# Kernel optimization log

Hardware: AMD Instinct MI355X
Metric: run time of the kernel (lower is better)

Reference implementation:

```python
import jax, jax.numpy as jnp
import numpy as np

G, NPG, C, H, F, L = 256, 128, 16, 128, 128, 3
N = G * NPG          # 32768 nodes
E = 524288           # 16 edges per node on average
REG, REG_C = 0.01, 0.01
LN_EPS = 1e-5


def setup_inputs() -> dict:
    key = jax.random.key(0)
    ks = jax.random.split(key, 20)
    x = jax.random.normal(ks[0], (N, F), dtype=jnp.float32)
    # edges kept within each graph so dense pooling matches to_dense_batch semantics
    epg = E // G
    offs = jnp.repeat(jnp.arange(G, dtype=jnp.int64) * NPG, epg)
    src = jax.random.randint(ks[1], (E,), 0, NPG, dtype=jnp.int64) + offs
    tgt = jax.random.randint(ks[2], (E,), 0, NPG, dtype=jnp.int64) + offs
    edge_index = jnp.stack([src, tgt])
    mask_breaks = jax.random.bernoulli(ks[3], 0.5, (E,))
    s = jax.random.uniform(ks[4], (N, C), dtype=jnp.float32)
    batch = jnp.repeat(jnp.arange(G, dtype=jnp.int64), NPG)
    sc = 1.0 / np.sqrt(H)
    Wn = jax.random.normal(ks[5], (L, H, H), dtype=jnp.float32) * sc
    bn_ = jax.random.normal(ks[6], (L, H), dtype=jnp.float32) * sc
    Wo = jax.random.normal(ks[7], (L, H, H), dtype=jnp.float32) * sc
    bo = jax.random.normal(ks[8], (L, H), dtype=jnp.float32) * sc
    Wr = jax.random.normal(ks[9], (L, H, H), dtype=jnp.float32) * sc
    ln_g = jnp.ones((L, H), dtype=jnp.float32)
    ln_b = jnp.zeros((L, H), dtype=jnp.float32)
    fln_g = jnp.ones((H,), dtype=jnp.float32)
    fln_b = jnp.zeros((H,), dtype=jnp.float32)
    lin_w = jax.random.normal(ks[10], (1, H), dtype=jnp.float32) * sc
    bias = jnp.zeros((1,), dtype=jnp.float32)
    return {"x": x, "edge_index": edge_index, "mask_breaks": mask_breaks, "s": s,
            "batch": batch, "Wn": Wn, "bn_": bn_, "Wo": Wo, "bo": bo, "Wr": Wr,
            "ln_g": ln_g, "ln_b": ln_b, "fln_g": fln_g, "fln_b": fln_b,
            "lin_w": lin_w, "bias": bias}


def _layernorm(h, g, b):
    mu = jnp.mean(h, axis=-1, keepdims=True)
    v = jnp.mean(jnp.square(h - mu), axis=-1, keepdims=True)
    return (h - mu) * jax.lax.rsqrt(v + LN_EPS) * g + b


def reference(x, edge_index, mask_breaks, s, batch, Wn, bn_, Wo, bo, Wr,
              ln_g, ln_b, fln_g, fln_b, lin_w, bias):
    src, tgt = edge_index[0], edge_index[1]
    ones_e = jnp.ones((E,), dtype=x.dtype)
    cnt = jax.ops.segment_sum(ones_e, tgt, num_segments=N)          # in-degree
    inv_cnt = (1.0 / jnp.maximum(cnt, 1.0))[:, None]
    h = x
    for i in range(L):
        x_in = h @ Wn[i].T + bn_[i]
        x_out = h @ Wo[i].T + bo[i]
        x_root = h @ Wr[i].T
        msg = jnp.where(mask_breaks[:, None], x_in[src], x_out[src])  # [E,H]
        agg = jax.ops.segment_sum(msg, tgt, num_segments=N) * inv_cnt  # mean aggr
        h = jax.nn.relu(_layernorm(agg + x_root, ln_g[i], ln_b[i]))
    # dense per-graph views (equal-size graphs, batch ids sorted -> reshape)
    xd = h.reshape(G, NPG, H)
    sd = s.reshape(G, NPG, C)
    pooled = jnp.einsum("gnc,gnh->gch", sd, xd)                      # [G,C,H]
    pooled = _layernorm(pooled, fln_g, fln_b)
    xc = pooled @ lin_w.T                                            # [G,C,1]
    col_sum = sd.sum(axis=1)                                          # [G,C]
    cmask = (col_sum > 0)[..., None]
    xc = xc * cmask.astype(xc.dtype)
    out = xc.sum(axis=1) + bias                                      # [G,1]
    reg_loss = jnp.abs(Wo).sum() + jnp.abs(bo).sum()
    denom = (cmask.astype(xc.dtype).squeeze(-1) + 1e-7).sum(axis=1, keepdims=True)
    l1_loss = (jnp.abs(xc).sum(axis=1) / denom).mean()
    losses = REG * reg_loss + REG_C * l1_loss
    return out, losses, xc
```

## Files before the change

### kernel.cpp

```cpp
#include <hip/hip_runtime.h>

#define NN   32768
#define HD   128
#define EE   524288
#define GG   256
#define EPG  2048
#define CCd  16
#define LLd  3

typedef short short8 __attribute__((ext_vector_type(8)));
typedef float f32x4 __attribute__((ext_vector_type(4)));

__device__ __forceinline__ unsigned short f2bf(float f) {
  unsigned u = __builtin_bit_cast(unsigned, f);
  return (unsigned short)((u + 0x7FFFu + ((u >> 16) & 1u)) >> 16);
}
__device__ __forceinline__ unsigned bfpack(float a, float b) {
  return (unsigned)f2bf(a) | ((unsigned)f2bf(b) << 16);
}

__global__ __launch_bounds__(256) void convert_w_kernel(const float* __restrict__ Wn, const float* __restrict__ Wo,
                                                        const float* __restrict__ Wr, const float* __restrict__ bo,
                                                        unsigned* __restrict__ Wnb, unsigned* __restrict__ Wob,
                                                        unsigned* __restrict__ Wrb, float* __restrict__ wsreg) {
  int i = blockIdx.x * 256 + threadIdx.x;
  float4 a = *(const float4*)(Wn + (size_t)i * 4);
  float4 b = *(const float4*)(Wo + (size_t)i * 4);
  float4 c = *(const float4*)(Wr + (size_t)i * 4);
  *(uint2*)(Wnb + (size_t)i * 2) = make_uint2(bfpack(a.x, a.y), bfpack(a.z, a.w));
  *(uint2*)(Wob + (size_t)i * 2) = make_uint2(bfpack(b.x, b.y), bfpack(b.z, b.w));
  *(uint2*)(Wrb + (size_t)i * 2) = make_uint2(bfpack(c.x, c.y), bfpack(c.z, c.w));
  float s = fabsf(b.x) + fabsf(b.y) + fabsf(b.z) + fabsf(b.w);
  if (blockIdx.x == 0 && threadIdx.x < 96) {
    float4 d = *(const float4*)(bo + threadIdx.x * 4);
    s += fabsf(d.x) + fabsf(d.y) + fabsf(d.z) + fabsf(d.w);
  }
#pragma unroll
  for (int mk = 1; mk < 64; mk <<= 1) s += __shfl_xor(s, mk, 64);
  if ((threadIdx.x & 63) == 0) atomicAdd(wsreg, s);
}

__global__ __launch_bounds__(256) void build_m_kernel(const int* __restrict__ src, const int* __restrict__ tgt,
                                                      const int* __restrict__ mask,
                                                      unsigned* __restrict__ Mb, float* __restrict__ fin,
                                                      float* __restrict__ fout) {
  __shared__ unsigned Mi[2 * 128 * 64];
  const int g = blockIdx.x;
  const int tid = threadIdx.x;
  for (int i = tid; i < 16384; i += 256) Mi[i] = 0;
  __syncthreads();
  const int e0 = g * EPG;
#pragma unroll
  for (int i = 0; i < 8; ++i) {
    int e = e0 + i * 256 + tid;
    int t = tgt[e] & 127;
    int sl = src[e] & 127;
    int dir = (mask[e] != 0) ? 0 : 1;
    atomicAdd(&Mi[dir * 8192 + t * 64 + (sl >> 1)], 1u << ((sl & 1) * 16));
  }
  __syncthreads();
  const int t = tid >> 1, p = tid & 1;
  unsigned nin = 0, nout = 0;
#pragma unroll 4
  for (int k = 0; k < 32; ++k) { unsigned v = Mi[t * 64 + p * 32 + k]; nin += (v & 0xffffu) + (v >> 16); }
#pragma unroll 4
  for (int k = 0; k < 32; ++k) { unsigned v = Mi[8192 + t * 64 + p * 32 + k]; nout += (v & 0xffffu) + (v >> 16); }
  nin += __shfl_xor((int)nin, 1);
  nout += __shfl_xor((int)nout, 1);
  unsigned dg = nin + nout;
  float inv = 1.0f / (float)(dg > 0 ? dg : 1);
  if (p == 0) { fin[g * 128 + t] = (float)nin * inv; fout[g * 128 + t] = (float)nout * inv; }
#pragma unroll
  for (int dir = 0; dir < 2; ++dir) {
    int base = dir * 8192 + t * 64 + p * 32;
#pragma unroll
    for (int k4 = 0; k4 < 8; ++k4) {
      uint4 v = *(const uint4*)&Mi[base + k4 * 4];
      uint4 o;
      o.x = bfpack((float)(v.x & 0xffffu) * inv, (float)(v.x >> 16) * inv);
      o.y = bfpack((float)(v.y & 0xffffu) * inv, (float)(v.y >> 16) * inv);
      o.z = bfpack((float)(v.z & 0xffffu) * inv, (float)(v.z >> 16) * inv);
      o.w = bfpack((float)(v.w & 0xffffu) * inv, (float)(v.w >> 16) * inv);
      *(uint4*)&Mb[(size_t)g * 16384 + base + k4 * 4] = o;
    }
  }
}

struct PF { uint4 a, b; };
__device__ __forceinline__ PF pf_load(const unsigned short* __restrict__ srcb, int tid) {
  int row = tid >> 2, c = tid & 3;
  const unsigned short* p = srcb + row * 128 + c * 8;
  PF r;
  r.a = *(const uint4*)p;
  r.b = *(const uint4*)(p + 32);
  return r;
}
__device__ __forceinline__ void pf_store(unsigned short* __restrict__ buf, const PF& r, int tid) {
  int row = tid >> 2, c = tid & 3;
  *(uint4*)(buf + row * 72 + c * 8) = r.a;
  *(uint4*)(buf + row * 72 + (c + 4) * 8) = r.b;
}
__device__ __forceinline__ const unsigned short* stage_ptr(int sIdx, const unsigned short* Mg,
                                                           const unsigned short* Wnb, const unsigned short* Wob,
                                                           const unsigned short* Wrb) {
  if (sIdx > 29) sIdx = 29;
  int L = sIdx / 10;
  int r = sIdx - L * 10;
  int half = r & 1;
  int op = r >> 1;
  const unsigned short* base;
  if (op == 0) base = Mg;
  else if (op == 1) base = Wnb + L * 16384;
  else if (op == 2) base = Mg + 16384;
  else if (op == 3) base = Wob + L * 16384;
  else base = Wrb + L * 16384;
  return base + half * 64;
}

__global__ __launch_bounds__(512) void fused_kernel(
    const float* __restrict__ x, const unsigned short* __restrict__ Mb,
    const unsigned short* __restrict__ Wnb, const unsigned short* __restrict__ Wob,
    const unsigned short* __restrict__ Wrb,
    const float* __restrict__ bn, const float* __restrict__ bo,
    const float* __restrict__ fin, const float* __restrict__ fout,
    const float* __restrict__ lng, const float* __restrict__ lnb,
    const float* __restrict__ s,
    const float* __restrict__ flng, const float* __restrict__ flnb,
    const float* __restrict__ linw, const float* __restrict__ bias,
    float* __restrict__ out, float* __restrict__ l1g) {
  __shared__ unsigned short hTs[128 * 136];
  __shared__ unsigned short sTs[16 * 136];
  __shared__ unsigned short buf[128 * 72];
  __shared__ float colsumS[CCd];
  __shared__ float xcs[CCd], axcs[CCd], msk[CCd];

  const int g = blockIdx.x;
  const int tid = threadIdx.x;
  const int wave = tid >> 6;
  const int lane = tid & 63;
  const int m = lane & 15;
  const int q = lane >> 4;
  const int t0 = wave << 4;
  const unsigned short* Mg = Mb + (size_t)g * 32768;

  int sIdx = 0;
  PF pf = pf_load(stage_ptr(0, Mg, Wnb, Wob, Wrb), tid);

  {
    const float4* xg = (const float4*)(x + (size_t)g * 16384);
#pragma unroll
    for (int i = 0; i < 8; ++i) {
      int flat = i * 512 + tid;
      int t = flat >> 5, f0 = (flat & 31) << 2;
      float4 v = xg[flat];
      hTs[(f0 + 0) * 136 + t] = f2bf(v.x);
      hTs[(f0 + 1) * 136 + t] = f2bf(v.y);
      hTs[(f0 + 2) * 136 + t] = f2bf(v.z);
      hTs[(f0 + 3) * 136 + t] = f2bf(v.w);
    }
    int t = tid >> 2, c0 = (tid & 3) << 2;
    float4 v = *(const float4*)(s + (size_t)g * 2048 + t * 16 + c0);
    sTs[(c0 + 0) * 136 + t] = f2bf(v.x);
    sTs[(c0 + 1) * 136 + t] = f2bf(v.y);
    sTs[(c0 + 2) * 136 + t] = f2bf(v.z);
    sTs[(c0 + 3) * 136 + t] = f2bf(v.w);
    if (tid < CCd) {
      float cs = 0.f;
      for (int tt = 0; tt < 128; ++tt) cs += s[(size_t)g * 2048 + tt * 16 + tid];
      colsumS[tid] = cs;
    }
  }

  for (int L = 0; L < LLd; ++L) {
    f32x4 pre[8];
#pragma unroll
    for (int ct = 0; ct < 8; ++ct) pre[ct] = (f32x4){0.f, 0.f, 0.f, 0.f};

    for (int sg = 0; sg < 2; ++sg) {
      f32x4 accT[8];
#pragma unroll
      for (int ft = 0; ft < 8; ++ft) accT[ft] = (f32x4){0.f, 0.f, 0.f, 0.f};
#pragma unroll
      for (int half = 0; half < 2; ++half) {
        __syncthreads();
        pf_store(buf, pf, tid);
        ++sIdx;
        pf = pf_load(stage_ptr(sIdx, Mg, Wnb, Wob, Wrb), tid);
        __syncthreads();
#pragma unroll
        for (int ksl = 0; ksl < 2; ++ksl) {
          const int ksg = half * 2 + ksl;
          short8 bfr = *(const short8*)&buf[(t0 + m) * 72 + ksl * 32 + q * 8];
#pragma unroll
          for (int ft = 0; ft < 8; ++ft) {
            short8 afr = *(const short8*)&hTs[(ft * 16 + m) * 136 + ksg * 32 + q * 8];
            accT[ft] = __builtin_amdgcn_mfma_f32_16x16x32_bf16(afr, bfr, accT[ft], 0, 0, 0);
          }
        }
      }
#pragma unroll
      for (int half = 0; half < 2; ++half) {
        __syncthreads();
        pf_store(buf, pf, tid);
        ++sIdx;
        pf = pf_load(stage_ptr(sIdx, Mg, Wnb, Wob, Wrb), tid);
        __syncthreads();
#pragma unroll
        for (int ksl = 0; ksl < 2; ++ksl) {
          const int ksg = half * 2 + ksl;
          f32x4 lo = accT[2 * ksg], hi = accT[2 * ksg + 1];
          short8 afr;
#pragma unroll
          for (int j = 0; j < 8; ++j) {
            int srcl = ((((q & 1) << 1) + (j >> 2)) << 4) + m;
            float ylo = __shfl(lo[j & 3], srcl, 64);
            float yhi = __shfl(hi[j & 3], srcl, 64);
            afr[j] = (short)f2bf((q >> 1) ? yhi : ylo);
          }
#pragma unroll
          for (int ct = 0; ct < 8; ++ct) {
            short8 bfr = *(const short8*)&buf[(ct * 16 + m) * 72 + ksl * 32 + q * 8];
            pre[ct] = __builtin_amdgcn_mfma_f32_16x16x32_bf16(afr, bfr, pre[ct], 0, 0, 0);
          }
        }
      }
    }
#pragma unroll
    for (int half = 0; half < 2; ++half) {
      __syncthreads();
      pf_store(buf, pf, tid);
      ++sIdx;
      pf = pf_load(stage_ptr(sIdx, Mg, Wnb, Wob, Wrb), tid);
      __syncthreads();
#pragma unroll
      for (int ksl = 0; ksl < 2; ++ksl) {
        const int ksg = half * 2 + ksl;
        short8 afr;
#pragma unroll
        for (int j = 0; j < 8; ++j)
          afr[j] = (short)hTs[(ksg * 32 + q * 8 + j) * 136 + t0 + m];
#pragma unroll
        for (int ct = 0; ct < 8; ++ct) {
          short8 bfr = *(const short8*)&buf[(ct * 16 + m) * 72 + ksl * 32 + q * 8];
          pre[ct] = __builtin_amdgcn_mfma_f32_16x16x32_bf16(afr, bfr, pre[ct], 0, 0, 0);
        }
      }
    }
    float bnv[8], bov[8], gv[8], bv[8];
#pragma unroll
    for (int ct = 0; ct < 8; ++ct) {
      int c = L * 128 + ct * 16 + m;
      bnv[ct] = bn[c]; bov[ct] = bo[c]; gv[ct] = lng[c]; bv[ct] = lnb[c];
    }
#pragma unroll
    for (int r = 0; r < 4; ++r) {
      const int tl = q * 4 + r;
      const int T = g * 128 + t0 + tl;
      const float fiv = fin[T], fov = fout[T];
      float v[8];
      float sum = 0.f;
#pragma unroll
      for (int ct = 0; ct < 8; ++ct) {
        v[ct] = pre[ct][r] + fiv * bnv[ct] + fov * bov[ct];
        sum += v[ct];
      }
      sum += __shfl_xor(sum, 1); sum += __shfl_xor(sum, 2);
      sum += __shfl_xor(sum, 4); sum += __shfl_xor(sum, 8);
      const float mu = sum * (1.0f / 128.0f);
      float sq = 0.f;
#pragma unroll
      for (int ct = 0; ct < 8; ++ct) { float d = v[ct] - mu; sq += d * d; }
      sq += __shfl_xor(sq, 1); sq += __shfl_xor(sq, 2);
      sq += __shfl_xor(sq, 4); sq += __shfl_xor(sq, 8);
      const float rstd = rsqrtf(sq * (1.0f / 128.0f) + 1e-5f);
#pragma unroll
      for (int ct = 0; ct < 8; ++ct) {
        float o = fmaxf((v[ct] - mu) * rstd * gv[ct] + bv[ct], 0.0f);
        hTs[(ct * 16 + m) * 136 + t0 + tl] = f2bf(o);
      }
    }
  }

  __syncthreads();
  f32x4 pl = (f32x4){0.f, 0.f, 0.f, 0.f};
#pragma unroll
  for (int ks = 0; ks < 4; ++ks) {
    short8 a = *(const short8*)&sTs[m * 136 + ks * 32 + q * 8];
    short8 b = *(const short8*)&hTs[(wave * 16 + m) * 136 + ks * 32 + q * 8];
    pl = __builtin_amdgcn_mfma_f32_16x16x32_bf16(a, b, pl, 0, 0, 0);
  }
  float* pooledS = (float*)buf;
#pragma unroll
  for (int r = 0; r < 4; ++r) pooledS[(q * 4 + r) * 132 + wave * 16 + m] = pl[r];
  __syncthreads();

  if (tid < 256) {
    const int c = tid >> 4;
    const int j0 = (tid & 15) << 3;
    float v[8];
#pragma unroll
    for (int jj = 0; jj < 8; ++jj) v[jj] = pooledS[c * 132 + j0 + jj];
    float sum = 0.f;
#pragma unroll
    for (int jj = 0; jj < 8; ++jj) sum += v[jj];
#pragma unroll
    for (int mk = 1; mk < 16; mk <<= 1) sum += __shfl_xor(sum, mk, 64);
    float mu = sum * (1.0f / 128.0f);
    float sq = 0.f;
#pragma unroll
    for (int jj = 0; jj < 8; ++jj) { float d = v[jj] - mu; sq += d * d; }
#pragma unroll
    for (int mk = 1; mk < 16; mk <<= 1) sq += __shfl_xor(sq, mk, 64);
    float rstd = rsqrtf(sq * (1.0f / 128.0f) + 1e-5f);
    float dot = 0.f;
#pragma unroll
    for (int jj = 0; jj < 8; ++jj) {
      float nv = (v[jj] - mu) * rstd * flng[j0 + jj] + flnb[j0 + jj];
      dot += nv * linw[j0 + jj];
    }
#pragma unroll
    for (int mk = 1; mk < 16; mk <<= 1) dot += __shfl_xor(dot, mk, 64);
    if ((tid & 15) == 0) {
      float cm = (colsumS[c] > 0.f) ? 1.0f : 0.0f;
      float xcv = dot * cm;
      out[257 + g * CCd + c] = xcv;
      xcs[c] = xcv; axcs[c] = fabsf(xcv); msk[c] = cm;
    }
  }
  __syncthreads();
  if (tid == 0) {
    float so = 0.f, sa = 0.f, sd = 0.f;
#pragma unroll
    for (int k = 0; k < CCd; ++k) { so += xcs[k]; sa += axcs[k]; sd += msk[k] + 1e-7f; }
    out[g] = so + bias[0];
    l1g[g] = sa / sd;
  }
}

__global__ __launch_bounds__(256) void combine_kernel(const float* __restrict__ l1g, const float* __restrict__ wsreg,
                                                      float* __restrict__ outp) {
  const int tid = threadIdx.x;
  float s2 = l1g[tid];
#pragma unroll
  for (int mk = 1; mk < 64; mk <<= 1) s2 += __shfl_xor(s2, mk, 64);
  __shared__ float rs2[4];
  if ((tid & 63) == 0) rs2[tid >> 6] = s2;
  __syncthreads();
  if (tid == 0) {
    float l1 = (rs2[0] + rs2[1] + rs2[2] + rs2[3]) * (1.0f / GG);
    outp[0] = 0.01f * wsreg[0] + 0.01f * l1;
  }
}

extern "C" void kernel_launch(void* const* d_in, const int* in_sizes, int n_in,
                              void* d_out, int out_size, void* d_ws, size_t ws_size,
                              hipStream_t stream) {
  (void)in_sizes; (void)n_in; (void)out_size; (void)ws_size;
  const float* x    = (const float*)d_in[0];
  const int*   ei   = (const int*)d_in[1];
  const int*   mask = (const int*)d_in[2];
  const float* s    = (const float*)d_in[3];
  const float* Wn   = (const float*)d_in[5];
  const float* bn   = (const float*)d_in[6];
  const float* Wo   = (const float*)d_in[7];
  const float* bo   = (const float*)d_in[8];
  const float* Wr   = (const float*)d_in[9];
  const float* lng  = (const float*)d_in[10];
  const float* lnb  = (const float*)d_in[11];
  const float* flng = (const float*)d_in[12];
  const float* flnb = (const float*)d_in[13];
  const float* linw = (const float*)d_in[14];
  const float* bias = (const float*)d_in[15];
  float* out = (float*)d_out;

  char* ws = (char*)d_ws;
  size_t off = 0;
  auto alloc = [&](size_t b) { char* p = ws + off; off += (b + 255) & ~(size_t)255; return p; };
  unsigned short* Mbuf = (unsigned short*)alloc((size_t)GG * 2 * 128 * 128 * 2);
  float* fin    = (float*)alloc((size_t)NN * 4);
  float* fout   = (float*)alloc((size_t)NN * 4);
  unsigned short* Wnb = (unsigned short*)alloc((size_t)LLd * HD * HD * 2);
  unsigned short* Wob = (unsigned short*)alloc((size_t)LLd * HD * HD * 2);
  unsigned short* Wrb = (unsigned short*)alloc((size_t)LLd * HD * HD * 2);
  float* l1g    = (float*)alloc((size_t)GG * 4);
  float* wsreg  = (float*)alloc(256);

  const int* srcA = ei;
  const int* tgtA = ei + EE;

  hipMemsetAsync(wsreg, 0, 4, stream);
  convert_w_kernel<<<LLd * HD * HD / (256 * 4), 256, 0, stream>>>(Wn, Wo, Wr, bo,
      (unsigned*)Wnb, (unsigned*)Wob, (unsigned*)Wrb, wsreg);
  build_m_kernel<<<GG, 256, 0, stream>>>(srcA, tgtA, mask, (unsigned*)Mbuf, fin, fout);
  fused_kernel<<<GG, 512, 0, stream>>>(x, Mbuf, Wnb, Wob, Wrb, bn, bo, fin, fout,
                                       lng, lnb, s, flng, flnb, linw, bias, out, l1g);
  combine_kernel<<<1, 256, 0, stream>>>(l1g, wsreg, out + 256);
}
```

Baseline: 160.3 us.

## Restructure per-layer GEMMs to read weights from global and stage Y chunks

Each layer's work changes shape. The hidden state now lives row-major in LDS. Weight fragments for Wr, Wn and Wo are loaded straight from global memory into registers, replacing the old LDS double-buffered prefetch pipeline and its ten synchronised stages. The Wn/Wo projections are computed in 32-node chunks, written to a small LDS buffer and multiplied by the aggregation matrix read directly from global, which removes the cross-lane shuffles used to reshape accumulators. The aim is fewer barriers and less LDS staging. The risk is exposed global-load latency, since there is no explicit prefetch, and a transposed strided LDS read in the final pooling step.

```diff
diff --git a/kernel.cpp b/kernel.cpp
--- a/kernel.cpp
+++ b/kernel.cpp
@@ -86,37 +86,8 @@
   }
 }
 
-struct PF { uint4 a, b; };
-__device__ __forceinline__ PF pf_load(const unsigned short* __restrict__ srcb, int tid) {
-  int row = tid >> 2, c = tid & 3;
-  const unsigned short* p = srcb + row * 128 + c * 8;
-  PF r;
-  r.a = *(const uint4*)p;
-  r.b = *(const uint4*)(p + 32);
-  return r;
-}
-__device__ __forceinline__ void pf_store(unsigned short* __restrict__ buf, const PF& r, int tid) {
-  int row = tid >> 2, c = tid & 3;
-  *(uint4*)(buf + row * 72 + c * 8) = r.a;
-  *(uint4*)(buf + row * 72 + (c + 4) * 8) = r.b;
-}
-__device__ __forceinline__ const unsigned short* stage_ptr(int sIdx, const unsigned short* Mg,
-                                                           const unsigned short* Wnb, const unsigned short* Wob,
-                                                           const unsigned short* Wrb) {
-  if (sIdx > 29) sIdx = 29;
-  int L = sIdx / 10;
-  int r = sIdx - L * 10;
-  int half = r & 1;
-  int op = r >> 1;
-  const unsigned short* base;
-  if (op == 0) base = Mg;
-  else if (op == 1) base = Wnb + L * 16384;
-  else if (op == 2) base = Mg + 16384;
-  else if (op == 3) base = Wob + L * 16384;
-  else base = Wrb + L * 16384;
-  return base + half * 64;
-}
-
+#define SSTR 136
+#define YSTR 40
 __global__ __launch_bounds__(512) void fused_kernel(
     const float* __restrict__ x, const unsigned short* __restrict__ Mb,
     const unsigned short* __restrict__ Wnb, const unsigned short* __restrict__ Wob,
@@ -128,9 +99,9 @@
     const float* __restrict__ flng, const float* __restrict__ flnb,
     const float* __restrict__ linw, const float* __restrict__ bias,
     float* __restrict__ out, float* __restrict__ l1g) {
-  __shared__ unsigned short hTs[128 * 136];
-  __shared__ unsigned short sTs[16 * 136];
-  __shared__ unsigned short buf[128 * 72];
+  __shared__ unsigned short scratch[128 * SSTR];
+  __shared__ unsigned short ys[2 * 128 * YSTR];
+  __shared__ unsigned short sTs[16 * SSTR];
   __shared__ float colsumS[CCd];
   __shared__ float xcs[CCd], axcs[CCd], msk[CCd];
 
@@ -140,112 +111,94 @@
   const int lane = tid & 63;
   const int m = lane & 15;
   const int q = lane >> 4;
-  const int t0 = wave << 4;
   const unsigned short* Mg = Mb + (size_t)g * 32768;
-
-  int sIdx = 0;
-  PF pf = pf_load(stage_ptr(0, Mg, Wnb, Wob, Wrb), tid);
+  unsigned* scratch32 = (unsigned*)scratch;
 
   {
     const float4* xg = (const float4*)(x + (size_t)g * 16384);
 #pragma unroll
     for (int i = 0; i < 8; ++i) {
       int flat = i * 512 + tid;
-      int t = flat >> 5, f0 = (flat & 31) << 2;
+      int t = flat >> 5, f = (flat & 31) << 2;
       float4 v = xg[flat];
-      hTs[(f0 + 0) * 136 + t] = f2bf(v.x);
-      hTs[(f0 + 1) * 136 + t] = f2bf(v.y);
-      hTs[(f0 + 2) * 136 + t] = f2bf(v.z);
-      hTs[(f0 + 3) * 136 + t] = f2bf(v.w);
+      int w0 = (t * SSTR + f) >> 1;
+      scratch32[w0] = bfpack(v.x, v.y);
+      scratch32[w0 + 1] = bfpack(v.z, v.w);
     }
     int t = tid >> 2, c0 = (tid & 3) << 2;
     float4 v = *(const float4*)(s + (size_t)g * 2048 + t * 16 + c0);
-    sTs[(c0 + 0) * 136 + t] = f2bf(v.x);
-    sTs[(c0 + 1) * 136 + t] = f2bf(v.y);
-    sTs[(c0 + 2) * 136 + t] = f2bf(v.z);
-    sTs[(c0 + 3) * 136 + t] = f2bf(v.w);
+    sTs[(c0 + 0) * SSTR + t] = f2bf(v.x);
+    sTs[(c0 + 1) * SSTR + t] = f2bf(v.y);
+    sTs[(c0 + 2) * SSTR + t] = f2bf(v.z);
+    sTs[(c0 + 3) * SSTR + t] = f2bf(v.w);
     if (tid < CCd) {
       float cs = 0.f;
       for (int tt = 0; tt < 128; ++tt) cs += s[(size_t)g * 2048 + tt * 16 + tid];
       colsumS[tid] = cs;
     }
   }
+  __syncthreads();
 
   for (int L = 0; L < LLd; ++L) {
+    const unsigned short* WnL = Wnb + (size_t)L * 16384;
+    const unsigned short* WoL = Wob + (size_t)L * 16384;
+    const unsigned short* WrL = Wrb + (size_t)L * 16384;
     f32x4 pre[8];
 #pragma unroll
     for (int ct = 0; ct < 8; ++ct) pre[ct] = (f32x4){0.f, 0.f, 0.f, 0.f};
 
-    for (int sg = 0; sg < 2; ++sg) {
-      f32x4 accT[8];
-#pragma unroll
-      for (int ft = 0; ft < 8; ++ft) accT[ft] = (f32x4){0.f, 0.f, 0.f, 0.f};
-#pragma unroll
-      for (int half = 0; half < 2; ++half) {
-        __syncthreads();
-        pf_store(buf, pf, tid);
-        ++sIdx;
-        pf = pf_load(stage_ptr(sIdx, Mg, Wnb, Wob, Wrb), tid);
-        __syncthreads();
-#pragma unroll
-        for (int ksl = 0; ksl < 2; ++ksl) {
-          const int ksg = half * 2 + ksl;
-          short8 bfr = *(const short8*)&buf[(t0 + m) * 72 + ksl * 32 + q * 8];
-#pragma unroll
-          for (int ft = 0; ft < 8; ++ft) {
-            short8 afr = *(const short8*)&hTs[(ft * 16 + m) * 136 + ksg * 32 + q * 8];
-            accT[ft] = __builtin_amdgcn_mfma_f32_16x16x32_bf16(afr, bfr, accT[ft], 0, 0, 0);
-          }
+#pragma unroll
+    for (int ks = 0; ks < 4; ++ks) {
+      short8 a = *(const short8*)&scratch[(wave * 16 + m) * SSTR + ks * 32 + q * 8];
+#pragma unroll
+      for (int ct = 0; ct < 8; ++ct) {
+        short8 b = *(const short8*)(WrL + (size_t)(ct * 16 + m) * 128 + ks * 32 + q * 8);
+        pre[ct] = __builtin_amdgcn_mfma_f32_16x16x32_bf16(a, b, pre[ct], 0, 0, 0);
+      }
+    }
+
+    short8 wnf[4], wof[4];
+#pragma unroll
+    for (int ks = 0; ks < 4; ++ks) {
+      wnf[ks] = *(const short8*)(WnL + (size_t)(wave * 16 + m) * 128 + ks * 32 + q * 8);
+      wof[ks] = *(const short8*)(WoL + (size_t)(wave * 16 + m) * 128 + ks * 32 + q * 8);
+    }
+
+    for (int sc = 0; sc < 4; ++sc) {
+      f32x4 ya[2][2];
+#pragma unroll
+      for (int o2 = 0; o2 < 2; ++o2)
+#pragma unroll
+        for (int st = 0; st < 2; ++st) ya[o2][st] = (f32x4){0.f, 0.f, 0.f, 0.f};
+#pragma unroll
+      for (int ks = 0; ks < 4; ++ks) {
+        short8 a0 = *(const short8*)&scratch[(sc * 32 + m) * SSTR + ks * 32 + q * 8];
+        short8 a1 = *(const short8*)&scratch[(sc * 32 + 16 + m) * SSTR + ks * 32 + q * 8];
+        ya[0][0] = __builtin_amdgcn_mfma_f32_16x16x32_bf16(a0, wnf[ks], ya[0][0], 0, 0, 0);
+        ya[0][1] = __builtin_amdgcn_mfma_f32_16x16x32_bf16(a1, wnf[ks], ya[0][1], 0, 0, 0);
+        ya[1][0] = __builtin_amdgcn_mfma_f32_16x16x32_bf16(a0, wof[ks], ya[1][0], 0, 0, 0);
+        ya[1][1] = __builtin_amdgcn_mfma_f32_16x16x32_bf16(a1, wof[ks], ya[1][1], 0, 0, 0);
+      }
+#pragma unroll
+      for (int o2 = 0; o2 < 2; ++o2)
+#pragma unroll
+        for (int st = 0; st < 2; ++st)
+#pragma unroll
+          for (int r = 0; r < 4; ++r)
+            ys[o2 * 128 * YSTR + (wave * 16 + m) * YSTR + st * 16 + q * 4 + r] = f2bf(ya[o2][st][r]);
+      __syncthreads();
+#pragma unroll
+      for (int o2 = 0; o2 < 2; ++o2) {
+        short8 am = *(const short8*)(Mg + (size_t)o2 * 16384 + (size_t)(wave * 16 + m) * 128 + sc * 32 + q * 8);
+#pragma unroll
+        for (int ct = 0; ct < 8; ++ct) {
+          short8 b = *(const short8*)&ys[o2 * 128 * YSTR + (ct * 16 + m) * YSTR + q * 8];
+          pre[ct] = __builtin_amdgcn_mfma_f32_16x16x32_bf16(am, b, pre[ct], 0, 0, 0);
         }
       }
-#pragma unroll
-      for (int half = 0; half < 2; ++half) {
-        __syncthreads();
-        pf_store(buf, pf, tid);
-        ++sIdx;
-        pf = pf_load(stage_ptr(sIdx, Mg, Wnb, Wob, Wrb), tid);
-        __syncthreads();
-#pragma unroll
-        for (int ksl = 0; ksl < 2; ++ksl) {
-          const int ksg = half * 2 + ksl;
-          f32x4 lo = accT[2 * ksg], hi = accT[2 * ksg + 1];
-          short8 afr;
-#pragma unroll
-          for (int j = 0; j < 8; ++j) {
-            int srcl = ((((q & 1) << 1) + (j >> 2)) << 4) + m;
-            float ylo = __shfl(lo[j & 3], srcl, 64);
-            float yhi = __shfl(hi[j & 3], srcl, 64);
-            afr[j] = (short)f2bf((q >> 1) ? yhi : ylo);
-          }
-#pragma unroll
-          for (int ct = 0; ct < 8; ++ct) {
-            short8 bfr = *(const short8*)&buf[(ct * 16 + m) * 72 + ksl * 32 + q * 8];
-            pre[ct] = __builtin_amdgcn_mfma_f32_16x16x32_bf16(afr, bfr, pre[ct], 0, 0, 0);
-          }
-        }
-      }
-    }
-#pragma unroll
-    for (int half = 0; half < 2; ++half) {
-      __syncthreads();
-      pf_store(buf, pf, tid);
-      ++sIdx;
-      pf = pf_load(stage_ptr(sIdx, Mg, Wnb, Wob, Wrb), tid);
-      __syncthreads();
-#pragma unroll
-      for (int ksl = 0; ksl < 2; ++ksl) {
-        const int ksg = half * 2 + ksl;
-        short8 afr;
-#pragma unroll
-        for (int j = 0; j < 8; ++j)
-          afr[j] = (short)hTs[(ksg * 32 + q * 8 + j) * 136 + t0 + m];
-#pragma unroll
-        for (int ct = 0; ct < 8; ++ct) {
-          short8 bfr = *(const short8*)&buf[(ct * 16 + m) * 72 + ksl * 32 + q * 8];
-          pre[ct] = __builtin_amdgcn_mfma_f32_16x16x32_bf16(afr, bfr, pre[ct], 0, 0, 0);
-        }
-      }
-    }
+      if (sc < 3) __syncthreads();
+    }
+
     float bnv[8], bov[8], gv[8], bv[8];
 #pragma unroll
     for (int ct = 0; ct < 8; ++ct) {
@@ -255,7 +208,7 @@
 #pragma unroll
     for (int r = 0; r < 4; ++r) {
       const int tl = q * 4 + r;
-      const int T = g * 128 + t0 + tl;
+      const int T = g * 128 + wave * 16 + tl;
       const float fiv = fin[T], fov = fout[T];
       float v[8];
       float sum = 0.f;
@@ -276,20 +229,23 @@
 #pragma unroll
       for (int ct = 0; ct < 8; ++ct) {
         float o = fmaxf((v[ct] - mu) * rstd * gv[ct] + bv[ct], 0.0f);
-        hTs[(ct * 16 + m) * 136 + t0 + tl] = f2bf(o);
-      }
-    }
-  }
-
-  __syncthreads();
+        scratch[(wave * 16 + tl) * SSTR + ct * 16 + m] = f2bf(o);
+      }
+    }
+    __syncthreads();
+  }
+
   f32x4 pl = (f32x4){0.f, 0.f, 0.f, 0.f};
 #pragma unroll
   for (int ks = 0; ks < 4; ++ks) {
-    short8 a = *(const short8*)&sTs[m * 136 + ks * 32 + q * 8];
-    short8 b = *(const short8*)&hTs[(wave * 16 + m) * 136 + ks * 32 + q * 8];
+    short8 a = *(const short8*)&sTs[m * SSTR + ks * 32 + q * 8];
+    short8 b;
+#pragma unroll
+    for (int j = 0; j < 8; ++j)
+      b[j] = (short)scratch[(ks * 32 + q * 8 + j) * SSTR + wave * 16 + m];
     pl = __builtin_amdgcn_mfma_f32_16x16x32_bf16(a, b, pl, 0, 0, 0);
   }
-  float* pooledS = (float*)buf;
+  float* pooledS = (float*)ys;
 #pragma unroll
   for (int r = 0; r < 4; ++r) pooledS[(q * 4 + r) * 132 + wave * 16 + m] = pl[r];
   __syncthreads();
```

New measurement: 163.7 us. +2.1%, slower.
